# Performance work log

Hardware: AMD Instinct MI355X
Metric: run time of the kernel (lower is better)

## Reference

```python
import jax, jax.numpy as jnp
import numpy as np

POOL_SIZES = (1, 3, 6, 8)
EPS = 1e-5


def conv1x1(x, W, b):
    # x: [b, cin, h, w], W: [cout, cin], b: [cout]
    return jnp.einsum('bchw,oc->bohw', x, W) + b[None, :, None, None]


def ppm(x):
    # x: [b, c, h, w] -> [b, c, S] with S = sum(p*p); H,W divisible by each p
    b, c, h, w = x.shape
    outs = []
    for p in POOL_SIZES:
        pooled = x.reshape(b, c, p, h // p, p, w // p).mean(axis=(3, 5))
        outs.append(pooled.reshape(b, c, p * p))
    return jnp.concatenate(outs, axis=-1)


def setup_inputs() -> dict:
    key = jax.random.key(0)
    ks = jax.random.split(key, 8)
    B, Cin, H, W = 4, 512, 120, 120
    Ck, Cv, Cout = 256, 256, 512
    x = jax.random.normal(ks[0], (B, Cin, H, W), dtype=jnp.float32)
    sc = lambda cin: 1.0 / np.sqrt(cin)
    Wk = jax.random.normal(ks[1], (Ck, Cin), dtype=jnp.float32) * sc(Cin)
    bk = jnp.zeros((Ck,), jnp.float32)
    gamma = jnp.ones((Ck,), jnp.float32)
    beta = jnp.zeros((Ck,), jnp.float32)
    mean = jax.random.normal(ks[2], (Ck,), dtype=jnp.float32) * 0.1
    var = jax.random.uniform(ks[3], (Ck,), dtype=jnp.float32, minval=0.5, maxval=1.5)
    Wv = jax.random.normal(ks[4], (Cv, Cin), dtype=jnp.float32) * sc(Cin)
    bv = jnp.zeros((Cv,), jnp.float32)
    # original inits Conv_Out to zero; use random weights for a nontrivial baseline
    Wo = jax.random.normal(ks[5], (Cout, Cv), dtype=jnp.float32) * sc(Cv)
    bo = jnp.zeros((Cout,), jnp.float32)
    return {'x': x, 'Wk': Wk, 'bk': bk, 'gamma': gamma, 'beta': beta,
            'mean': mean, 'var': var, 'Wv': Wv, 'bv': bv, 'Wo': Wo, 'bo': bo}


def reference(x, Wk, bk, gamma, beta, mean, var, Wv, bv, Wo, bo):
    b, _, h, w = x.shape
    ck = Wk.shape[0]
    cv = Wv.shape[0]
    # shared Conv_Key / Conv_Query: conv1x1 -> BN (inference) -> ReLU
    kq = conv1x1(x, Wk, bk)
    inv = gamma / jnp.sqrt(var + EPS)
    kq = jax.nn.relu(kq * inv[None, :, None, None] + (beta - mean * inv)[None, :, None, None])
    value = ppm(conv1x1(x, Wv, bv)).transpose(0, 2, 1)      # [b, S, cv]
    key = ppm(kq)                                            # [b, ck, S]
    query = kq.reshape(b, ck, h * w).transpose(0, 2, 1)      # [b, hw, ck]
    scores = jnp.einsum('bnc,bcs->bns', query, key) * (ck ** -0.5)
    attn = jax.nn.softmax(scores, axis=-1)                   # [b, hw, S]
    agg = jnp.einsum('bns,bsv->bnv', attn, value)            # [b, hw, cv]
    agg = agg.transpose(0, 2, 1).reshape(b, cv, h, w)
    return conv1x1(agg, Wo, bo)
```

## Files before the change

kernel.cpp:

```cpp
#include <hip/hip_runtime.h>
#include <cstdint>
#include <cstddef>

#define HW 14400
#define WIDTH 120
#define S_TOT 110

typedef unsigned short u16;
typedef __attribute__((ext_vector_type(8))) short bf16x8;
typedef __attribute__((ext_vector_type(4))) float f32x4;

__device__ __forceinline__ u16 f2bf(float x) {
  unsigned u = __float_as_uint(x);
  unsigned r = (u + 0x7fffu + ((u >> 16) & 1u)) >> 16;
  return (u16)r;
}
__device__ __forceinline__ float bf2f(u16 h) {
  return __uint_as_float((unsigned)h << 16);
}

__device__ __forceinline__ void async16(void* lds, const void* g) {
  __builtin_amdgcn_global_load_lds(
      (const __attribute__((address_space(1))) void*)g,
      (__attribute__((address_space(3))) void*)lds, 16, 0, 0);
}

__global__ __launch_bounds__(256) void pool_kernel(const float* __restrict__ in,
                                                   float* __restrict__ outp) {
  __shared__ float colsum[2880];
  __shared__ float part[576];
  const float* plane = in + (size_t)blockIdx.x * HW;
  int t = threadIdx.x;
  for (int i = t; i < 2880; i += 256) {
    int by = i / 120, x = i - by * 120;
    const float* p0 = plane + (by * 5) * WIDTH + x;
    colsum[i] = p0[0] + p0[WIDTH] + p0[2 * WIDTH] + p0[3 * WIDTH] + p0[4 * WIDTH];
  }
  __syncthreads();
  for (int bb = t; bb < 576; bb += 256) {
    int by = bb / 24, bx = bb - by * 24;
    const float* c = &colsum[by * 120 + bx * 5];
    part[bb] = c[0] + c[1] + c[2] + c[3] + c[4];
  }
  __syncthreads();
  if (t < S_TOT) {
    float s = 0.f;
    if (t == 0) {
      for (int i = 0; i < 576; ++i) s += part[i];
      s *= (1.f / 14400.f);
    } else if (t < 10) {
      int idx = t - 1, i = idx / 3, j = idx % 3;
      for (int a = 0; a < 8; ++a)
        for (int c = 0; c < 8; ++c) s += part[(i * 8 + a) * 24 + (j * 8 + c)];
      s *= (1.f / 1600.f);
    } else if (t < 46) {
      int idx = t - 10, i = idx / 6, j = idx % 6;
      for (int a = 0; a < 4; ++a)
        for (int c = 0; c < 4; ++c) s += part[(i * 4 + a) * 24 + (j * 4 + c)];
      s *= (1.f / 400.f);
    } else {
      int idx = t - 46, i = idx / 8, j = idx % 8;
      for (int a = 0; a < 3; ++a)
        for (int c = 0; c < 3; ++c) s += part[(i * 3 + a) * 24 + (j * 3 + c)];
      s *= (1.f / 225.f);
    }
    outp[(size_t)blockIdx.x * S_TOT + t] = s;
  }
}

__global__ __launch_bounds__(256) void convert_w(const float* __restrict__ in,
                                                 u16* __restrict__ hi,
                                                 u16* __restrict__ lo, int n) {
  int i = blockIdx.x * 256 + threadIdx.x;
  if (i < n) {
    float v = in[i];
    u16 h = f2bf(v);
    hi[i] = h;
    lo[i] = f2bf(v - bf2f(h));
  }
}

template <int CIN>
__global__ __launch_bounds__(256) void convert_t(const float* __restrict__ X,
                                                 u16* __restrict__ xth,
                                                 u16* __restrict__ xtl) {
  __shared__ float ls[64][65];
  int b = blockIdx.z;
  int n0 = blockIdx.x * 64, k0 = blockIdx.y * 64;
  int t = threadIdx.x;
  int rt = t >> 4, c4 = (t & 15) * 4;
#pragma unroll
  for (int rr = 0; rr < 4; ++rr) {
    int kk = rr * 16 + rt;
    float4 v = *(const float4*)&X[((size_t)(b * CIN + k0 + kk)) * HW + n0 + c4];
    ls[kk][c4] = v.x; ls[kk][c4 + 1] = v.y; ls[kk][c4 + 2] = v.z; ls[kk][c4 + 3] = v.w;
  }
  __syncthreads();
#pragma unroll
  for (int rr = 0; rr < 4; ++rr) {
    int nn = rr * 16 + rt;
    float v0 = ls[c4 + 0][nn], v1 = ls[c4 + 1][nn], v2 = ls[c4 + 2][nn], v3 = ls[c4 + 3][nn];
    ushort4 oh, ol;
    oh.x = f2bf(v0); ol.x = f2bf(v0 - bf2f(oh.x));
    oh.y = f2bf(v1); ol.y = f2bf(v1 - bf2f(oh.y));
    oh.z = f2bf(v2); ol.z = f2bf(v2 - bf2f(oh.z));
    oh.w = f2bf(v3); ol.w = f2bf(v3 - bf2f(oh.w));
    size_t idx = ((size_t)(b * HW + n0 + nn)) * CIN + k0 + c4;
    *(ushort4*)&xth[idx] = oh;
    *(ushort4*)&xtl[idx] = ol;
  }
}

template <int K, int M_TOT, bool BNRELU>
__global__ __launch_bounds__(512, 2) void gemm_mfma(
    const u16* __restrict__ Ah, const u16* __restrict__ Al,
    const u16* __restrict__ Bh, const u16* __restrict__ Bl,
    float* __restrict__ C,
    const float* __restrict__ p0, const float* __restrict__ p1,
    const float* __restrict__ p2, const float* __restrict__ p3,
    const float* __restrict__ p4,
    u16* __restrict__ Th, u16* __restrict__ Tl) {
  constexpr int NSTEP = K / 32;
  __shared__ alignas(16) u16 smem[61440];

  int t = threadIdx.x, w = t >> 6, l = t & 63;
  int wm = w >> 2, wn = w & 3;
  int b = blockIdx.z;
  int n0 = blockIdx.x * 192;
  int m0 = blockIdx.y * 128;

  int fr = l & 15, fkc = l >> 4;
  const size_t bOff = (size_t)b * HW;

  auto stage = [&](int ks, int slot) {
    int k0 = ks * 32;
#pragma unroll
    for (int c = 0; c < 5; ++c) {
      int i = w * 5 + c;
      const u16* g;
      u16* d;
      if (i < 8) {
        g = Ah + (size_t)(m0 + i * 16 + fr) * K + k0 + fkc * 8;
        d = &smem[slot * 8192 + i * 512];
      } else if (i < 16) {
        g = Al + (size_t)(m0 + (i - 8) * 16 + fr) * K + k0 + fkc * 8;
        d = &smem[slot * 8192 + i * 512];
      } else if (i < 28) {
        g = Bh + (bOff + n0 + (i - 16) * 16 + fr) * (size_t)K + k0 + fkc * 8;
        d = &smem[24576 + slot * 12288 + (i - 16) * 512];
      } else {
        g = Bl + (bOff + n0 + (i - 28) * 16 + fr) * (size_t)K + k0 + fkc * 8;
        d = &smem[24576 + slot * 12288 + (i - 16) * 512];
      }
      async16(d, g);
    }
  };

  f32x4 acc[4][3];
#pragma unroll
  for (int i = 0; i < 4; ++i)
#pragma unroll
    for (int j = 0; j < 3; ++j) acc[i][j] = (f32x4){0.f, 0.f, 0.f, 0.f};

  stage(0, 0);
  stage(1, 1);

  for (int ks = 0; ks < NSTEP; ++ks) {
    if (ks + 1 < NSTEP)
      asm volatile("s_waitcnt vmcnt(5)" ::: "memory");
    else
      asm volatile("s_waitcnt vmcnt(0)" ::: "memory");
    __builtin_amdgcn_s_barrier();
    __builtin_amdgcn_sched_barrier(0);

    if (ks + 2 < NSTEP) stage(ks + 2, (ks + 2) % 3);

    int cur = ks % 3;
    bf16x8 bh[3], bl[3];
#pragma unroll
    for (int nt = 0; nt < 3; ++nt) {
      bh[nt] = *(const bf16x8*)&smem[24576 + cur * 12288 + (wn * 3 + nt) * 512 + l * 8];
      bl[nt] = *(const bf16x8*)&smem[24576 + cur * 12288 + (12 + wn * 3 + nt) * 512 + l * 8];
    }
    bf16x8 ah[4], al[4];
#pragma unroll
    for (int mt = 0; mt < 4; ++mt) {
      ah[mt] = *(const bf16x8*)&smem[cur * 8192 + (wm * 4 + mt) * 512 + l * 8];
      al[mt] = *(const bf16x8*)&smem[cur * 8192 + (8 + wm * 4 + mt) * 512 + l * 8];
    }
    __builtin_amdgcn_s_setprio(1);
#pragma unroll
    for (int mt = 0; mt < 4; ++mt)
#pragma unroll
      for (int nt = 0; nt < 3; ++nt) {
        acc[mt][nt] = __builtin_amdgcn_mfma_f32_16x16x32_bf16(ah[mt], bh[nt], acc[mt][nt], 0, 0, 0);
        acc[mt][nt] = __builtin_amdgcn_mfma_f32_16x16x32_bf16(ah[mt], bl[nt], acc[mt][nt], 0, 0, 0);
        acc[mt][nt] = __builtin_amdgcn_mfma_f32_16x16x32_bf16(al[mt], bh[nt], acc[mt][nt], 0, 0, 0);
      }
    __builtin_amdgcn_s_setprio(0);
  }

  __syncthreads();

  int q4 = (l >> 4) * 4;
#pragma unroll
  for (int mt = 0; mt < 4; ++mt) {
    int mb = m0 + (wm * 4 + mt) * 16 + q4;
    float iv[4], ad[4];
    if (BNRELU) {
      float4 g0 = *(const float4*)&p0[mb];
      float4 g1 = *(const float4*)&p1[mb];
      float4 g2 = *(const float4*)&p2[mb];
      float4 g3 = *(const float4*)&p3[mb];
      float4 g4 = *(const float4*)&p4[mb];
      iv[0] = g1.x * rsqrtf(g4.x + 1e-5f);
      iv[1] = g1.y * rsqrtf(g4.y + 1e-5f);
      iv[2] = g1.z * rsqrtf(g4.z + 1e-5f);
      iv[3] = g1.w * rsqrtf(g4.w + 1e-5f);
      ad[0] = (g0.x - g3.x) * iv[0] + g2.x;
      ad[1] = (g0.y - g3.y) * iv[1] + g2.y;
      ad[2] = (g0.z - g3.z) * iv[2] + g2.z;
      ad[3] = (g0.w - g3.w) * iv[3] + g2.w;
    } else {
      float4 g0 = *(const float4*)&p0[mb];
      ad[0] = g0.x; ad[1] = g0.y; ad[2] = g0.z; ad[3] = g0.w;
    }
#pragma unroll
    for (int nt = 0; nt < 3; ++nt) {
      int n = n0 + (wn * 3 + nt) * 16 + fr;
      float v[4];
#pragma unroll
      for (int r = 0; r < 4; ++r) {
        float x = acc[mt][nt][r];
        v[r] = BNRELU ? fmaxf(x * iv[r] + ad[r], 0.f) : x + ad[r];
        C[((size_t)(b * M_TOT) + mb + r) * HW + n] = v[r];
      }
      if (BNRELU && Th) {
        ushort4 hh, ll;
        hh.x = f2bf(v[0]); ll.x = f2bf(v[0] - bf2f(hh.x));
        hh.y = f2bf(v[1]); ll.y = f2bf(v[1] - bf2f(hh.y));
        hh.z = f2bf(v[2]); ll.z = f2bf(v[2] - bf2f(hh.z));
        hh.w = f2bf(v[3]); ll.w = f2bf(v[3] - bf2f(hh.w));
        int nl = (wn * 3 + nt) * 16 + fr;
        int ml = (wm * 4 + mt) * 16 + q4;
        *(ushort4*)&smem[nl * 136 + ml] = hh;
        *(ushort4*)&smem[26112 + nl * 136 + ml] = ll;
      }
    }
  }
  if (BNRELU && Th) {
    __syncthreads();
#pragma unroll
    for (int it = 0; it < 6; ++it) {
      int row = it * 32 + (t >> 4);
      int c8 = (t & 15) * 8;
      size_t go = (bOff + n0 + row) * (size_t)M_TOT + m0 + c8;
      *(bf16x8*)&Th[go] = *(const bf16x8*)&smem[row * 136 + c8];
      *(bf16x8*)&Tl[go] = *(const bf16x8*)&smem[26112 + row * 136 + c8];
    }
  }
}

__global__ __launch_bounds__(256) void value_kernel(
    const float* __restrict__ Wv, const float* __restrict__ xp,
    const float* __restrict__ bv, u16* __restrict__ vth,
    u16* __restrict__ vtl) {
  int b = blockIdx.x >> 7, s = blockIdx.x & 127;
  int t = threadIdx.x;
  size_t o = ((size_t)(b * 256 + t)) * 128 + s;
  if (s >= S_TOT) { vth[o] = 0; vtl[o] = 0; return; }
  __shared__ float xs[512];
  for (int i = t; i < 512; i += 256) xs[i] = xp[((size_t)b * 512 + i) * S_TOT + s];
  __syncthreads();
  float accv = 0.f;
  const float* wv = Wv + (size_t)t * 512;
  for (int k = 0; k < 512; k += 4) {
    float4 w4 = *(const float4*)&wv[k];
    accv += w4.x * xs[k] + w4.y * xs[k + 1] + w4.z * xs[k + 2] + w4.w * xs[k + 3];
  }
  accv += bv[t];
  u16 h = f2bf(accv);
  vth[o] = h;
  vtl[o] = f2bf(accv - bf2f(h));
}

__global__ __launch_bounds__(256) void convert_key(const float* __restrict__ keyp,
                                                   u16* __restrict__ kth,
                                                   u16* __restrict__ ktl) {
  int b = blockIdx.x;
  int t = threadIdx.x;
  for (int i = t; i < 128 * 256; i += 256) {
    int s = i >> 8, c = i & 255;
    float v = (s < S_TOT) ? keyp[((size_t)(b * 256 + c)) * S_TOT + s] : 0.f;
    u16 h = f2bf(v);
    size_t o = ((size_t)(b * 128 + s)) * 256 + c;
    kth[o] = h;
    ktl[o] = f2bf(v - bf2f(h));
  }
}

__global__ __launch_bounds__(256) void attn_mfma(
    const u16* __restrict__ qh, const u16* __restrict__ ql,
    const u16* __restrict__ kh, const u16* __restrict__ kl,
    const u16* __restrict__ vh, const u16* __restrict__ vl,
    u16* __restrict__ aggh, u16* __restrict__ aggl) {
  __shared__ alignas(16) u16 lds[17408];
  int b = blockIdx.y, pix0 = blockIdx.x * 64;
  int t = threadIdx.x, w = t >> 6, l = t & 63;
  int fr = l & 15, q = l >> 4;

  const u16* kbase_h = kh + (size_t)b * 128 * 256;
  const u16* kbase_l = kl + (size_t)b * 128 * 256;

  f32x4 acc[8];
#pragma unroll
  for (int st = 0; st < 8; ++st) acc[st] = (f32x4){0.f, 0.f, 0.f, 0.f};

  const u16* qbh = qh + ((size_t)(b * HW + pix0 + w * 16 + fr)) * 256 + q * 8;
  const u16* qbl = ql + ((size_t)(b * HW + pix0 + w * 16 + fr)) * 256 + q * 8;

  auto stageK = [&](int ks, int buf) {
    int c0 = ks * 32;
#pragma unroll
    for (int j = 0; j < 4; ++j) {
      int i = t + j * 256;
      int half = i >> 9;
      int idx = i & 511;
      int st = idx >> 6, ll = idx & 63;
      const u16* src = (half ? kbase_l : kbase_h) +
                       (st * 16 + (ll & 15)) * 256 + c0 + (ll >> 4) * 8;
      async16(&lds[buf * 8192 + half * 4096 + idx * 8], src);
    }
  };

  stageK(0, 0);
  for (int ks = 0; ks < 8; ++ks) {
    __syncthreads();
    if (ks < 7) stageK(ks + 1, (ks + 1) & 1);
    bf16x8 ah = *(const bf16x8*)(qbh + ks * 32);
    bf16x8 al = *(const bf16x8*)(qbl + ks * 32);
    const u16* kb = &lds[(ks & 1) * 8192 + l * 8];
#pragma unroll
    for (int st = 0; st < 8; ++st) {
      bf16x8 bh = *(const bf16x8*)(kb + st * 512);
      bf16x8 bl = *(const bf16x8*)(kb + 4096 + st * 512);
      acc[st] = __builtin_amdgcn_mfma_f32_16x16x32_bf16(ah, bh, acc[st], 0, 0, 0);
      acc[st] = __builtin_amdgcn_mfma_f32_16x16x32_bf16(ah, bl, acc[st], 0, 0, 0);
      acc[st] = __builtin_amdgcn_mfma_f32_16x16x32_bf16(al, bh, acc[st], 0, 0, 0);
    }
  }

#pragma unroll
  for (int st = 0; st < 8; ++st)
#pragma unroll
    for (int r = 0; r < 4; ++r) acc[st][r] *= 0.0625f;
  if (fr >= 14) {
#pragma unroll
    for (int r = 0; r < 4; ++r) acc[6][r] = -1e30f;
  }
#pragma unroll
  for (int r = 0; r < 4; ++r) acc[7][r] = -1e30f;

#pragma unroll
  for (int r = 0; r < 4; ++r) {
    float m = -1e30f;
#pragma unroll
    for (int st = 0; st < 8; ++st) m = fmaxf(m, acc[st][r]);
    m = fmaxf(m, __shfl_xor(m, 1));
    m = fmaxf(m, __shfl_xor(m, 2));
    m = fmaxf(m, __shfl_xor(m, 4));
    m = fmaxf(m, __shfl_xor(m, 8));
    float s = 0.f;
#pragma unroll
    for (int st = 0; st < 8; ++st) {
      float e = __expf(acc[st][r] - m);
      acc[st][r] = e;
      s += e;
    }
    s += __shfl_xor(s, 1);
    s += __shfl_xor(s, 2);
    s += __shfl_xor(s, 4);
    s += __shfl_xor(s, 8);
    float inv = 1.f / s;
#pragma unroll
    for (int st = 0; st < 8; ++st) acc[st][r] *= inv;
  }

  __syncthreads();

  int prow = w * 16 + q * 4;
#pragma unroll
  for (int st = 0; st < 8; ++st) {
    int s = st * 16 + fr;
#pragma unroll
    for (int r = 0; r < 4; ++r) {
      float v = acc[st][r];
      u16 h = f2bf(v);
      lds[(prow + r) * 136 + s] = h;
      lds[8704 + (prow + r) * 136 + s] = f2bf(v - bf2f(h));
    }
  }
  __syncthreads();

  f32x4 oacc[4][4];
#pragma unroll
  for (int nt = 0; nt < 4; ++nt)
#pragma unroll
    for (int pt = 0; pt < 4; ++pt) oacc[nt][pt] = (f32x4){0.f, 0.f, 0.f, 0.f};

  const u16* vbh = vh + ((size_t)(b * 256 + w * 64 + fr)) * 128 + q * 8;
  const u16* vbl = vl + ((size_t)(b * 256 + w * 64 + fr)) * 128 + q * 8;

#pragma unroll
  for (int kc = 0; kc < 4; ++kc) {
    bf16x8 ph[4], pl[4];
#pragma unroll
    for (int pt = 0; pt < 4; ++pt) {
      ph[pt] = *(const bf16x8*)&lds[(pt * 16 + fr) * 136 + kc * 32 + q * 8];
      pl[pt] = *(const bf16x8*)&lds[8704 + (pt * 16 + fr) * 136 + kc * 32 + q * 8];
    }
#pragma unroll
    for (int nt = 0; nt < 4; ++nt) {
      bf16x8 a_h = *(const bf16x8*)(vbh + (size_t)nt * 16 * 128 + kc * 32);
      bf16x8 a_l = *(const bf16x8*)(vbl + (size_t)nt * 16 * 128 + kc * 32);
#pragma unroll
      for (int pt = 0; pt < 4; ++pt) {
        oacc[nt][pt] = __builtin_amdgcn_mfma_f32_16x16x32_bf16(a_h, ph[pt], oacc[nt][pt], 0, 0, 0);
        oacc[nt][pt] = __builtin_amdgcn_mfma_f32_16x16x32_bf16(a_h, pl[pt], oacc[nt][pt], 0, 0, 0);
        oacc[nt][pt] = __builtin_amdgcn_mfma_f32_16x16x32_bf16(a_l, ph[pt], oacc[nt][pt], 0, 0, 0);
      }
    }
  }

#pragma unroll
  for (int nt = 0; nt < 4; ++nt) {
#pragma unroll
    for (int pt = 0; pt < 4; ++pt) {
      ushort4 oh, ol;
      float v0 = oacc[nt][pt][0], v1 = oacc[nt][pt][1];
      float v2 = oacc[nt][pt][2], v3 = oacc[nt][pt][3];
      oh.x = f2bf(v0); ol.x = f2bf(v0 - bf2f(oh.x));
      oh.y = f2bf(v1); ol.y = f2bf(v1 - bf2f(oh.y));
      oh.z = f2bf(v2); ol.z = f2bf(v2 - bf2f(oh.z));
      oh.w = f2bf(v3); ol.w = f2bf(v3 - bf2f(oh.w));
      size_t o = ((size_t)(b * HW + pix0 + pt * 16 + fr)) * 256 + (w * 4 + nt) * 16 + q * 4;
      *(ushort4*)&aggh[o] = oh;
      *(ushort4*)&aggl[o] = ol;
    }
  }
}

extern "C" void kernel_launch(void* const* d_in, const int* in_sizes, int n_in,
                              void* d_out, int out_size, void* d_ws, size_t ws_size,
                              hipStream_t stream) {
  (void)in_sizes; (void)n_in; (void)out_size;
  const float* x     = (const float*)d_in[0];
  const float* Wk    = (const float*)d_in[1];
  const float* bk    = (const float*)d_in[2];
  const float* gamma = (const float*)d_in[3];
  const float* beta  = (const float*)d_in[4];
  const float* mean  = (const float*)d_in[5];
  const float* var   = (const float*)d_in[6];
  const float* Wv    = (const float*)d_in[7];
  const float* bv    = (const float*)d_in[8];
  const float* Wo    = (const float*)d_in[9];
  const float* bo    = (const float*)d_in[10];
  float* out = (float*)d_out;

  char* p = (char*)d_ws;
  float* kq = (float*)p;      p += (size_t)14745600 * 4;
  u16* xth = (u16*)p;         p += (size_t)29491200 * 2;
  u16* xtl = (u16*)p;         p += (size_t)29491200 * 2;
  u16* wkh = (u16*)p;         p += 131072 * 2;
  u16* wkl = (u16*)p;         p += 131072 * 2;
  u16* woh = (u16*)p;         p += 131072 * 2;
  u16* wol = (u16*)p;         p += 131072 * 2;
  float* xp = (float*)p;      p += (size_t)4 * 512 * 110 * 4;
  float* keyp = (float*)p;    p += (size_t)4 * 256 * 110 * 4;
  u16* vth = (u16*)p;         p += (size_t)4 * 256 * 128 * 2;
  u16* vtl = (u16*)p;         p += (size_t)4 * 256 * 128 * 2;
  u16* kth = (u16*)p;         p += (size_t)4 * 128 * 256 * 2;
  u16* ktl = (u16*)p;         p += (size_t)4 * 128 * 256 * 2;
  u16* kqth_f = (u16*)p;      p += (size_t)14745600 * 2;
  u16* kqtl_f = (u16*)p;      p += (size_t)14745600 * 2;
  bool fused = ((size_t)(p - (char*)d_ws) <= ws_size);

  u16* aggh = xth;
  u16* aggl = xtl;
  u16* kqth = fused ? kqth_f : xth + (size_t)14745600;
  u16* kqtl = fused ? kqtl_f : xtl + (size_t)14745600;

  convert_w<<<512, 256, 0, stream>>>(Wk, wkh, wkl, 256 * 512);
  convert_w<<<512, 256, 0, stream>>>(Wo, woh, wol, 512 * 256);
  convert_t<512><<<dim3(225, 8, 4), 256, 0, stream>>>(x, xth, xtl);
  pool_kernel<<<dim3(4 * 512), dim3(256), 0, stream>>>(x, xp);
  value_kernel<<<dim3(4 * 128), dim3(256), 0, stream>>>(Wv, xp, bv, vth, vtl);
  gemm_mfma<512, 256, true><<<dim3(75, 2, 4), 512, 0, stream>>>(
      wkh, wkl, xth, xtl, kq, bk, gamma, beta, mean, var,
      fused ? kqth : (u16*)nullptr, fused ? kqtl : (u16*)nullptr);
  if (!fused)
    convert_t<256><<<dim3(225, 4, 4), 256, 0, stream>>>(kq, kqth, kqtl);
  pool_kernel<<<dim3(4 * 256), dim3(256), 0, stream>>>(kq, keyp);
  convert_key<<<dim3(4), dim3(256), 0, stream>>>(keyp, kth, ktl);
  attn_mfma<<<dim3(225, 4), 256, 0, stream>>>(kqth, kqtl, kth, ktl, vth, vtl,
                                              aggh, aggl);
  gemm_mfma<256, 512, false><<<dim3(75, 4, 4), 512, 0, stream>>>(
      woh, wol, aggh, aggl, out, bo, nullptr, nullptr, nullptr, nullptr,
      nullptr, nullptr);
}
```

Measured before the change: 557.3 us.

## Fuse pyramid pooling into transpose and key GEMM epilogues via atomics

Pyramid pooling sums are now accumulated with atomicAdd inside the input transpose kernel and inside the key GEMM epilogue, reading from LDS-staged tiles, so the standalone pool passes over x and kq disappear. In the fused path the GEMM no longer writes the fp32 kq tensor at all, which removes a large global write. Pooled sums are stored in an [S, C] layout and scaled by region size when consumed. The cost is many global atomics, memset launches, and float-order nondeterminism in the pooled sums. The fallback path passes summed buffers to a kernel that writes means, which looks mismatched but only runs when workspace is short.

```diff
diff --git a/kernel.cpp b/kernel.cpp
--- a/kernel.cpp
+++ b/kernel.cpp
@@ -23,6 +23,13 @@
   __builtin_amdgcn_global_load_lds(
       (const __attribute__((address_space(1))) void*)g,
       (__attribute__((address_space(3))) void*)lds, 16, 0, 0);
+}
+
+__device__ __forceinline__ float pool_scale(int s) {
+  return (s == 0) ? (1.f / 14400.f)
+         : (s < 10) ? (1.f / 1600.f)
+         : (s < 46) ? (1.f / 400.f)
+                    : (1.f / 225.f);
 }
 
 __global__ __launch_bounds__(256) void pool_kernel(const float* __restrict__ in,
@@ -83,7 +90,8 @@
 template <int CIN>
 __global__ __launch_bounds__(256) void convert_t(const float* __restrict__ X,
                                                  u16* __restrict__ xth,
-                                                 u16* __restrict__ xtl) {
+                                                 u16* __restrict__ xtl,
+                                                 float* __restrict__ psum) {
   __shared__ float ls[64][65];
   int b = blockIdx.z;
   int n0 = blockIdx.x * 64, k0 = blockIdx.y * 64;
@@ -109,6 +117,32 @@
     *(ushort4*)&xth[idx] = oh;
     *(ushort4*)&xtl[idx] = ol;
   }
+  if (psum) {
+    int c = t & 63, g = t >> 6;
+    float s1 = 0.f, s3 = 0.f, s6 = 0.f, s8 = 0.f;
+    int b3 = -1, b6 = -1, b8 = -1;
+    float* base = psum + (size_t)b * 110 * CIN + k0 + c;
+    for (int i = 0; i < 16; ++i) {
+      int px = g * 16 + i;
+      int n = n0 + px;
+      int row = n / 120, col = n - row * 120;
+      int i3 = 1 + (row / 40) * 3 + col / 40;
+      int i6 = 10 + (row / 20) * 6 + col / 20;
+      int i8 = 46 + (row / 15) * 8 + col / 15;
+      float v = ls[c][px];
+      s1 += v;
+      if (i3 != b3) { if (b3 >= 0) atomicAdd(base + (size_t)b3 * CIN, s3); s3 = 0.f; b3 = i3; }
+      s3 += v;
+      if (i6 != b6) { if (b6 >= 0) atomicAdd(base + (size_t)b6 * CIN, s6); s6 = 0.f; b6 = i6; }
+      s6 += v;
+      if (i8 != b8) { if (b8 >= 0) atomicAdd(base + (size_t)b8 * CIN, s8); s8 = 0.f; b8 = i8; }
+      s8 += v;
+    }
+    atomicAdd(base, s1);
+    atomicAdd(base + (size_t)b3 * CIN, s3);
+    atomicAdd(base + (size_t)b6 * CIN, s6);
+    atomicAdd(base + (size_t)b8 * CIN, s8);
+  }
 }
 
 template <int K, int M_TOT, bool BNRELU>
@@ -119,7 +153,8 @@
     const float* __restrict__ p0, const float* __restrict__ p1,
     const float* __restrict__ p2, const float* __restrict__ p3,
     const float* __restrict__ p4,
-    u16* __restrict__ Th, u16* __restrict__ Tl) {
+    u16* __restrict__ Th, u16* __restrict__ Tl,
+    float* __restrict__ PS) {
   constexpr int NSTEP = K / 32;
   __shared__ alignas(16) u16 smem[61440];
 
@@ -233,7 +268,7 @@
       for (int r = 0; r < 4; ++r) {
         float x = acc[mt][nt][r];
         v[r] = BNRELU ? fmaxf(x * iv[r] + ad[r], 0.f) : x + ad[r];
-        C[((size_t)(b * M_TOT) + mb + r) * HW + n] = v[r];
+        if (C) C[((size_t)(b * M_TOT) + mb + r) * HW + n] = v[r];
       }
       if (BNRELU && Th) {
         ushort4 hh, ll;
@@ -258,19 +293,47 @@
       *(bf16x8*)&Th[go] = *(const bf16x8*)&smem[row * 136 + c8];
       *(bf16x8*)&Tl[go] = *(const bf16x8*)&smem[26112 + row * 136 + c8];
     }
+    if (PS) {
+      int c = t & 127, g = t >> 7;
+      float s1 = 0.f, s3 = 0.f, s6 = 0.f, s8 = 0.f;
+      int b3 = -1, b6 = -1, b8 = -1;
+      float* base = PS + (size_t)b * 110 * M_TOT + m0 + c;
+      for (int i = 0; i < 48; ++i) {
+        int px = g * 48 + i;
+        int n = n0 + px;
+        int row = n / 120, col = n - row * 120;
+        int i3 = 1 + (row / 40) * 3 + col / 40;
+        int i6 = 10 + (row / 20) * 6 + col / 20;
+        int i8 = 46 + (row / 15) * 8 + col / 15;
+        float v = bf2f(smem[px * 136 + c]) + bf2f(smem[26112 + px * 136 + c]);
+        s1 += v;
+        if (i3 != b3) { if (b3 >= 0) atomicAdd(base + (size_t)b3 * M_TOT, s3); s3 = 0.f; b3 = i3; }
+        s3 += v;
+        if (i6 != b6) { if (b6 >= 0) atomicAdd(base + (size_t)b6 * M_TOT, s6); s6 = 0.f; b6 = i6; }
+        s6 += v;
+        if (i8 != b8) { if (b8 >= 0) atomicAdd(base + (size_t)b8 * M_TOT, s8); s8 = 0.f; b8 = i8; }
+        s8 += v;
+      }
+      atomicAdd(base, s1);
+      atomicAdd(base + (size_t)b3 * M_TOT, s3);
+      atomicAdd(base + (size_t)b6 * M_TOT, s6);
+      atomicAdd(base + (size_t)b8 * M_TOT, s8);
+    }
   }
 }
 
 __global__ __launch_bounds__(256) void value_kernel(
-    const float* __restrict__ Wv, const float* __restrict__ xp,
+    const float* __restrict__ Wv, const float* __restrict__ xpsum,
     const float* __restrict__ bv, u16* __restrict__ vth,
     u16* __restrict__ vtl) {
   int b = blockIdx.x >> 7, s = blockIdx.x & 127;
   int t = threadIdx.x;
   size_t o = ((size_t)(b * 256 + t)) * 128 + s;
   if (s >= S_TOT) { vth[o] = 0; vtl[o] = 0; return; }
+  float scale = pool_scale(s);
   __shared__ float xs[512];
-  for (int i = t; i < 512; i += 256) xs[i] = xp[((size_t)b * 512 + i) * S_TOT + s];
+  for (int i = t; i < 512; i += 256)
+    xs[i] = xpsum[((size_t)b * 110 + s) * 512 + i] * scale;
   __syncthreads();
   float accv = 0.f;
   const float* wv = Wv + (size_t)t * 512;
@@ -284,6 +347,7 @@
   vtl[o] = f2bf(accv - bf2f(h));
 }
 
+template <int SUMLAYOUT>
 __global__ __launch_bounds__(256) void convert_key(const float* __restrict__ keyp,
                                                    u16* __restrict__ kth,
                                                    u16* __restrict__ ktl) {
@@ -291,7 +355,13 @@
   int t = threadIdx.x;
   for (int i = t; i < 128 * 256; i += 256) {
     int s = i >> 8, c = i & 255;
-    float v = (s < S_TOT) ? keyp[((size_t)(b * 256 + c)) * S_TOT + s] : 0.f;
+    float v = 0.f;
+    if (s < S_TOT) {
+      if (SUMLAYOUT)
+        v = keyp[((size_t)(b * 110 + s)) * 256 + c] * pool_scale(s);
+      else
+        v = keyp[((size_t)(b * 256 + c)) * S_TOT + s];
+    }
     u16 h = f2bf(v);
     size_t o = ((size_t)(b * 128 + s)) * 256 + c;
     kth[o] = h;
@@ -475,8 +545,8 @@
   u16* wkl = (u16*)p;         p += 131072 * 2;
   u16* woh = (u16*)p;         p += 131072 * 2;
   u16* wol = (u16*)p;         p += 131072 * 2;
-  float* xp = (float*)p;      p += (size_t)4 * 512 * 110 * 4;
-  float* keyp = (float*)p;    p += (size_t)4 * 256 * 110 * 4;
+  float* xpsum = (float*)p;   p += (size_t)4 * 110 * 512 * 4;
+  float* keypsum = (float*)p; p += (size_t)4 * 110 * 256 * 4;
   u16* vth = (u16*)p;         p += (size_t)4 * 256 * 128 * 2;
   u16* vtl = (u16*)p;         p += (size_t)4 * 256 * 128 * 2;
   u16* kth = (u16*)p;         p += (size_t)4 * 128 * 256 * 2;
@@ -490,21 +560,27 @@
   u16* kqth = fused ? kqth_f : xth + (size_t)14745600;
   u16* kqtl = fused ? kqtl_f : xtl + (size_t)14745600;
 
+  hipMemsetAsync(xpsum, 0, (size_t)4 * 110 * 512 * 4, stream);
+  hipMemsetAsync(keypsum, 0, (size_t)4 * 110 * 256 * 4, stream);
+
   convert_w<<<512, 256, 0, stream>>>(Wk, wkh, wkl, 256 * 512);
   convert_w<<<512, 256, 0, stream>>>(Wo, woh, wol, 512 * 256);
-  convert_t<512><<<dim3(225, 8, 4), 256, 0, stream>>>(x, xth, xtl);
-  pool_kernel<<<dim3(4 * 512), dim3(256), 0, stream>>>(x, xp);
-  value_kernel<<<dim3(4 * 128), dim3(256), 0, stream>>>(Wv, xp, bv, vth, vtl);
+  convert_t<512><<<dim3(225, 8, 4), 256, 0, stream>>>(x, xth, xtl, xpsum);
+  value_kernel<<<dim3(4 * 128), 256, 0, stream>>>(Wv, xpsum, bv, vth, vtl);
   gemm_mfma<512, 256, true><<<dim3(75, 2, 4), 512, 0, stream>>>(
-      wkh, wkl, xth, xtl, kq, bk, gamma, beta, mean, var,
-      fused ? kqth : (u16*)nullptr, fused ? kqtl : (u16*)nullptr);
-  if (!fused)
-    convert_t<256><<<dim3(225, 4, 4), 256, 0, stream>>>(kq, kqth, kqtl);
-  pool_kernel<<<dim3(4 * 256), dim3(256), 0, stream>>>(kq, keyp);
-  convert_key<<<dim3(4), dim3(256), 0, stream>>>(keyp, kth, ktl);
+      wkh, wkl, xth, xtl, fused ? nullptr : kq, bk, gamma, beta, mean, var,
+      fused ? kqth : (u16*)nullptr, fused ? kqtl : (u16*)nullptr,
+      fused ? keypsum : (float*)nullptr);
+  if (!fused) {
+    convert_t<256><<<dim3(225, 4, 4), 256, 0, stream>>>(kq, kqth, kqtl, nullptr);
+    pool_kernel<<<dim3(4 * 256), dim3(256), 0, stream>>>(kq, keypsum);
+    convert_key<0><<<dim3(4), dim3(256), 0, stream>>>(keypsum, kth, ktl);
+  } else {
+    convert_key<1><<<dim3(4), dim3(256), 0, stream>>>(keypsum, kth, ktl);
+  }
   attn_mfma<<<dim3(225, 4), 256, 0, stream>>>(kqth, kqtl, kth, ktl, vth, vtl,
                                               aggh, aggl);
   gemm_mfma<256, 512, false><<<dim3(75, 4, 4), 512, 0, stream>>>(
       woh, wol, aggh, aggl, out, bo, nullptr, nullptr, nullptr, nullptr,
-      nullptr, nullptr);
-}
+      nullptr, nullptr, nullptr);
+}
```

Result: slower. 590.5 us (+6.0%).

## Drop fp32 key-query store and pool keys from transposed bf16 split with atomics

Applied to the files above, without the earlier changes.

When the fused path is available, the key GEMM no longer writes its fp32 output. The key pooling now reads the transposed bf16 hi/lo copy through a new banded kernel that accumulates partial sums with atomicAdd into a zeroed [S, C] buffer. Scaling by pool area is moved into convert_key. This removes a roughly 59 MB fp32 write and its re-read, at the cost of a memset, atomic traffic and pooled keys rebuilt from the bf16 hi+lo pair.

```diff
diff --git a/kernel.cpp b/kernel.cpp
--- a/kernel.cpp
+++ b/kernel.cpp
@@ -23,6 +23,13 @@
   __builtin_amdgcn_global_load_lds(
       (const __attribute__((address_space(1))) void*)g,
       (__attribute__((address_space(3))) void*)lds, 16, 0, 0);
+}
+
+__device__ __forceinline__ float pool_scale(int s) {
+  return (s == 0) ? (1.f / 14400.f)
+         : (s < 10) ? (1.f / 1600.f)
+         : (s < 46) ? (1.f / 400.f)
+                    : (1.f / 225.f);
 }
 
 __global__ __launch_bounds__(256) void pool_kernel(const float* __restrict__ in,
@@ -233,7 +240,7 @@
       for (int r = 0; r < 4; ++r) {
         float x = acc[mt][nt][r];
         v[r] = BNRELU ? fmaxf(x * iv[r] + ad[r], 0.f) : x + ad[r];
-        C[((size_t)(b * M_TOT) + mb + r) * HW + n] = v[r];
+        if (C) C[((size_t)(b * M_TOT) + mb + r) * HW + n] = v[r];
       }
       if (BNRELU && Th) {
         ushort4 hh, ll;
@@ -261,6 +268,41 @@
   }
 }
 
+__global__ __launch_bounds__(256) void pool_kqt(const u16* __restrict__ kqth,
+                                                const u16* __restrict__ kqtl,
+                                                float* __restrict__ keypsum) {
+  int cq = blockIdx.x, band = blockIdx.y, b = blockIdx.z;
+  int t = threadIdx.x;
+  int row0 = band * 5, col0 = cq * 30;
+  int r3 = row0 / 40, r6 = row0 / 20, r8 = row0 / 15;
+  float* base = keypsum + (size_t)b * 110 * 256 + t;
+  float s1 = 0.f, s3 = 0.f, s6 = 0.f, s8 = 0.f;
+  int b3 = -1, b6 = -1, b8 = -1;
+  for (int cc = 0; cc < 30; ++cc) {
+    int col = col0 + cc;
+    float v = 0.f;
+#pragma unroll
+    for (int r = 0; r < 5; ++r) {
+      size_t o = ((size_t)(b * HW + (row0 + r) * 120 + col)) * 256 + t;
+      v += bf2f(kqth[o]) + bf2f(kqtl[o]);
+    }
+    int i3 = 1 + r3 * 3 + col / 40;
+    int i6 = 10 + r6 * 6 + col / 20;
+    int i8 = 46 + r8 * 8 + col / 15;
+    s1 += v;
+    if (i3 != b3) { if (b3 >= 0) atomicAdd(base + (size_t)b3 * 256, s3); s3 = 0.f; b3 = i3; }
+    s3 += v;
+    if (i6 != b6) { if (b6 >= 0) atomicAdd(base + (size_t)b6 * 256, s6); s6 = 0.f; b6 = i6; }
+    s6 += v;
+    if (i8 != b8) { if (b8 >= 0) atomicAdd(base + (size_t)b8 * 256, s8); s8 = 0.f; b8 = i8; }
+    s8 += v;
+  }
+  atomicAdd(base, s1);
+  atomicAdd(base + (size_t)b3 * 256, s3);
+  atomicAdd(base + (size_t)b6 * 256, s6);
+  atomicAdd(base + (size_t)b8 * 256, s8);
+}
+
 __global__ __launch_bounds__(256) void value_kernel(
     const float* __restrict__ Wv, const float* __restrict__ xp,
     const float* __restrict__ bv, u16* __restrict__ vth,
@@ -284,6 +326,7 @@
   vtl[o] = f2bf(accv - bf2f(h));
 }
 
+template <int SUMLAYOUT>
 __global__ __launch_bounds__(256) void convert_key(const float* __restrict__ keyp,
                                                    u16* __restrict__ kth,
                                                    u16* __restrict__ ktl) {
@@ -291,7 +334,13 @@
   int t = threadIdx.x;
   for (int i = t; i < 128 * 256; i += 256) {
     int s = i >> 8, c = i & 255;
-    float v = (s < S_TOT) ? keyp[((size_t)(b * 256 + c)) * S_TOT + s] : 0.f;
+    float v = 0.f;
+    if (s < S_TOT) {
+      if (SUMLAYOUT)
+        v = keyp[((size_t)(b * 110 + s)) * 256 + c] * pool_scale(s);
+      else
+        v = keyp[((size_t)(b * 256 + c)) * S_TOT + s];
+    }
     u16 h = f2bf(v);
     size_t o = ((size_t)(b * 128 + s)) * 256 + c;
     kth[o] = h;
@@ -476,7 +525,7 @@
   u16* woh = (u16*)p;         p += 131072 * 2;
   u16* wol = (u16*)p;         p += 131072 * 2;
   float* xp = (float*)p;      p += (size_t)4 * 512 * 110 * 4;
-  float* keyp = (float*)p;    p += (size_t)4 * 256 * 110 * 4;
+  float* keypsum = (float*)p; p += (size_t)4 * 110 * 256 * 4;
   u16* vth = (u16*)p;         p += (size_t)4 * 256 * 128 * 2;
   u16* vtl = (u16*)p;         p += (size_t)4 * 256 * 128 * 2;
   u16* kth = (u16*)p;         p += (size_t)4 * 128 * 256 * 2;
@@ -490,18 +539,25 @@
   u16* kqth = fused ? kqth_f : xth + (size_t)14745600;
   u16* kqtl = fused ? kqtl_f : xtl + (size_t)14745600;
 
+  if (fused)
+    hipMemsetAsync(keypsum, 0, (size_t)4 * 110 * 256 * 4, stream);
+
   convert_w<<<512, 256, 0, stream>>>(Wk, wkh, wkl, 256 * 512);
   convert_w<<<512, 256, 0, stream>>>(Wo, woh, wol, 512 * 256);
   convert_t<512><<<dim3(225, 8, 4), 256, 0, stream>>>(x, xth, xtl);
   pool_kernel<<<dim3(4 * 512), dim3(256), 0, stream>>>(x, xp);
-  value_kernel<<<dim3(4 * 128), dim3(256), 0, stream>>>(Wv, xp, bv, vth, vtl);
+  value_kernel<<<dim3(4 * 128), 256, 0, stream>>>(Wv, xp, bv, vth, vtl);
   gemm_mfma<512, 256, true><<<dim3(75, 2, 4), 512, 0, stream>>>(
-      wkh, wkl, xth, xtl, kq, bk, gamma, beta, mean, var,
+      wkh, wkl, xth, xtl, fused ? nullptr : kq, bk, gamma, beta, mean, var,
       fused ? kqth : (u16*)nullptr, fused ? kqtl : (u16*)nullptr);
-  if (!fused)
+  if (fused) {
+    pool_kqt<<<dim3(4, 24, 4), 256, 0, stream>>>(kqth, kqtl, keypsum);
+    convert_key<1><<<dim3(4), dim3(256), 0, stream>>>(keypsum, kth, ktl);
+  } else {
     convert_t<256><<<dim3(225, 4, 4), 256, 0, stream>>>(kq, kqth, kqtl);
-  pool_kernel<<<dim3(4 * 256), dim3(256), 0, stream>>>(kq, keyp);
-  convert_key<<<dim3(4), dim3(256), 0, stream>>>(keyp, kth, ktl);
+    pool_kernel<<<dim3(4 * 256), dim3(256), 0, stream>>>(kq, keypsum);
+    convert_key<0><<<dim3(4), dim3(256), 0, stream>>>(keypsum, kth, ktl);
+  }
   attn_mfma<<<dim3(225, 4), 256, 0, stream>>>(kqth, kqtl, kth, ktl, vth, vtl,
                                               aggh, aggl);
   gemm_mfma<256, 512, false><<<dim3(75, 4, 4), 512, 0, stream>>>(
```

Result: no change. 566.3 us (+1.6%).
